# Optimization experiments

Hardware: AMD Instinct MI355X
Metric: run time of the kernel (lower is better)

## Reference

```python
import jax, jax.numpy as jnp
import numpy as np

D_MODEL = 1024
N_HEADS = 16
D_K = D_MODEL // N_HEADS


def _rope_sin_cos(seq_len, d_k, dtype):
    inv_freq = 1.0 / (10000.0 ** (jnp.arange(0, d_k, 2, dtype=jnp.float32) / d_k))
    pos = jnp.arange(seq_len, dtype=jnp.float32)[:, None]          # [S,1]
    ang = pos * inv_freq[None, :]                                   # [S,d_k/2]
    sin = jnp.concatenate([jnp.sin(ang), jnp.sin(ang)], axis=-1)    # [S,d_k]
    cos = jnp.concatenate([jnp.cos(ang), jnp.cos(ang)], axis=-1)
    return sin.astype(dtype), cos.astype(dtype)


def _rotate_half(x):
    x1, x2 = jnp.split(x, 2, axis=-1)
    return jnp.concatenate([-x2, x1], axis=-1)


def _apply_rope(x, sin, cos):
    # x: [B,H,S,d_k]; sin/cos: [S,d_k] broadcast over B,H
    return x * cos[None, None] + _rotate_half(x) * sin[None, None]


def setup_inputs() -> dict:
    key = jax.random.key(0)
    ks = jax.random.split(key, 8)
    B, S = 2, 2048
    s = 1.0 / np.sqrt(D_MODEL)
    return {
        "query": jax.random.normal(ks[0], (B, S, D_MODEL), jnp.float32),
        "key": jax.random.normal(ks[1], (B, S, D_MODEL), jnp.float32),
        "value": jax.random.normal(ks[2], (B, S, D_MODEL), jnp.float32),
        "Wq": jax.random.normal(ks[3], (D_MODEL, D_MODEL), jnp.float32) * s,
        "Wk": jax.random.normal(ks[4], (D_MODEL, D_MODEL), jnp.float32) * s,
        "Wv": jax.random.normal(ks[5], (D_MODEL, D_MODEL), jnp.float32) * s,
        "Wo": jax.random.normal(ks[6], (D_MODEL, D_MODEL), jnp.float32) * s,
        "bo": jnp.zeros((D_MODEL,), jnp.float32),
    }


def reference(query, key, value, Wq, Wk, Wv, Wo, bo):
    B, Sq, _ = query.shape
    Sk = key.shape[1]
    # projections; torch Linear: x @ W.T (here W stored as [out,in])
    Q = (query @ Wq.T).reshape(B, Sq, N_HEADS, D_K).transpose(0, 2, 1, 3)
    K = (key @ Wk.T).reshape(B, Sk, N_HEADS, D_K).transpose(0, 2, 1, 3)
    V = (value @ Wv.T).reshape(B, Sk, N_HEADS, D_K).transpose(0, 2, 1, 3)
    sin_q, cos_q = _rope_sin_cos(Sq, D_K, Q.dtype)
    sin_k, cos_k = _rope_sin_cos(Sk, D_K, K.dtype)
    Q = _apply_rope(Q, sin_q, cos_q)
    K = _apply_rope(K, sin_k, cos_k)
    scores = jnp.einsum("bhqd,bhkd->bhqk", Q, K) / jnp.sqrt(jnp.asarray(D_K, Q.dtype))
    attn = jax.nn.softmax(scores, axis=-1)
    ctx = jnp.einsum("bhqk,bhkd->bhqd", attn, V)
    ctx = ctx.transpose(0, 2, 1, 3).reshape(B, Sq, D_MODEL)
    out = ctx @ Wo.T + bo
    return out, attn
```

## Files before the change

kernel.cpp:

```cpp
#include <hip/hip_runtime.h>
#include <cmath>

#define BB 2
#define SS 2048
#define DMODEL 1024
#define NHEADS 16
#define DK 64
#define BSR (BB*SS)

typedef float f32x4 __attribute__((ext_vector_type(4)));
typedef short s16x8 __attribute__((ext_vector_type(8)));
typedef unsigned short ushort_t;
#define MFMA_BF16 __builtin_amdgcn_mfma_f32_16x16x32_bf16

__device__ __forceinline__ unsigned short f2bf(float x) {
    unsigned int u = __float_as_uint(x);
    unsigned int r = u + 0x7FFFu + ((u >> 16) & 1u);
    return (unsigned short)(r >> 16);
}
__device__ __forceinline__ float bf2f(unsigned short h) {
    return __uint_as_float(((unsigned int)h) << 16);
}
__device__ __forceinline__ unsigned int pk2(float lo, float hi) {
    return (unsigned int)f2bf(lo) | ((unsigned int)f2bf(hi) << 16);
}

__device__ __forceinline__ size_t qk_idx(int bh, int s, int d) {
    return ((((size_t)bh * 128 + (s >> 4)) * 2 + (d >> 5)) * 4 + ((d >> 3) & 3)) * 128
           + (size_t)((s & 15) * 8 + (d & 7));
}
__device__ __forceinline__ size_t v_idx(int bh, int s, int d) {
    return ((((size_t)bh * 64 + (s >> 5)) * 4 + (d >> 4)) * 4 + ((s >> 3) & 3)) * 128
           + (size_t)((d & 15) * 8 + (s & 7));
}

__global__ __launch_bounds__(256)
void split_tab(const float* __restrict__ q, const float* __restrict__ k,
               const float* __restrict__ v, const float* __restrict__ wq,
               const float* __restrict__ wk, const float* __restrict__ wv,
               const float* __restrict__ wo,
               ushort_t* qsh, ushort_t* qsl, ushort_t* ksh, ushort_t* ksl,
               ushort_t* vsh, ushort_t* vsl,
               ushort_t* wqh, ushort_t* wql, ushort_t* wkh, ushort_t* wkl,
               ushort_t* wvh, ushort_t* wvl, ushort_t* woh, ushort_t* wol,
               float2* __restrict__ tab)
{
    int blk = blockIdx.x;
    if (blk >= 8192) {
        const int t = (blk - 8192) * 256 + threadIdx.x;
        const int s = t >> 5, j = t & 31;
        const double l2 = 13.287712379549449 / 32.0;
        const float invf = (float)exp2(-(double)j * l2);
        const float ang = (float)s * invf;
        tab[t] = make_float2(cosf(ang), sinf(ang));
        return;
    }
    const float* src; ushort_t* dh; ushort_t* dl;
    if      (blk < 2048) { src = q;  dh = qsh; dl = qsl; }
    else if (blk < 4096) { src = k;  dh = ksh; dl = ksl; blk -= 2048; }
    else if (blk < 6144) { src = v;  dh = vsh; dl = vsl; blk -= 4096; }
    else if (blk < 6656) { src = wq; dh = wqh; dl = wql; blk -= 6144; }
    else if (blk < 7168) { src = wk; dh = wkh; dl = wkl; blk -= 6656; }
    else if (blk < 7680) { src = wv; dh = wvh; dl = wvl; blk -= 7168; }
    else                 { src = wo; dh = woh; dl = wol; blk -= 7680; }
    const size_t off = (size_t)blk * 2048 + threadIdx.x * 8;
    float4 a = *reinterpret_cast<const float4*>(src + off);
    float4 b = *reinterpret_cast<const float4*>(src + off + 4);
    float xs[8] = {a.x, a.y, a.z, a.w, b.x, b.y, b.z, b.w};
    s16x8 hi, lo;
#pragma unroll
    for (int i = 0; i < 8; ++i) {
        unsigned short h = f2bf(xs[i]);
        hi[i] = (short)h;
        lo[i] = (short)f2bf(xs[i] - bf2f(h));
    }
    *reinterpret_cast<s16x8*>(dh + off) = hi;
    *reinterpret_cast<s16x8*>(dl + off) = lo;
}

__global__ __launch_bounds__(256)
void qkv_gemm(const ushort_t* __restrict__ qsh, const ushort_t* __restrict__ qsl,
              const ushort_t* __restrict__ ksh, const ushort_t* __restrict__ ksl,
              const ushort_t* __restrict__ vsh, const ushort_t* __restrict__ vsl,
              const ushort_t* __restrict__ wqh, const ushort_t* __restrict__ wql,
              const ushort_t* __restrict__ wkh, const ushort_t* __restrict__ wkl,
              const ushort_t* __restrict__ wvh, const ushort_t* __restrict__ wvl,
              ushort_t* __restrict__ Qhi, ushort_t* __restrict__ Qlo,
              ushort_t* __restrict__ Khi, ushort_t* __restrict__ Klo,
              ushort_t* __restrict__ Vt,
              const float2* __restrict__ tab)
{
    __shared__ __align__(16) ushort_t smAh[128 * 64];
    __shared__ __align__(16) ushort_t smAl[128 * 64];
    __shared__ __align__(16) ushort_t smBh[64 * 64];
    __shared__ __align__(16) ushort_t smBl[64 * 64];

    const int tid = threadIdx.x;
    const int lane = tid & 63;
    const int w = tid >> 6;
    const int lane16 = lane & 15;
    const int grp = (lane >> 4) & 3;
    const int m0 = blockIdx.y * 128;
    const int n0 = blockIdx.x * 64;
    const int z  = blockIdx.z;
    const int K = 1024;

    const ushort_t* Ah = (z == 0) ? vsh : ((z == 1) ? qsh : ksh);
    const ushort_t* Al = (z == 0) ? vsl : ((z == 1) ? qsl : ksl);
    const ushort_t* Bh = (z == 0) ? wvh : ((z == 1) ? wqh : wkh);
    const ushort_t* Bl = (z == 0) ? wvl : ((z == 1) ? wql : wkl);

    f32x4 acc[2][4];
#pragma unroll
    for (int a = 0; a < 2; ++a)
#pragma unroll
        for (int e = 0; e < 4; ++e) acc[a][e] = (f32x4){0.f, 0.f, 0.f, 0.f};

    for (int k0 = 0; k0 < K; k0 += 64) {
#pragma unroll
        for (int i = 0; i < 4; ++i) {
            const int c = tid + 256 * i;
            const int row = c >> 3, gs = c & 7;
            const int dst = row * 64 + ((gs ^ (row & 7)) * 8);
            const size_t src = (size_t)(m0 + row) * K + k0 + gs * 8;
            *reinterpret_cast<s16x8*>(&smAh[dst]) = *reinterpret_cast<const s16x8*>(&Ah[src]);
            *reinterpret_cast<s16x8*>(&smAl[dst]) = *reinterpret_cast<const s16x8*>(&Al[src]);
        }
#pragma unroll
        for (int i = 0; i < 2; ++i) {
            const int c = tid + 256 * i;
            const int row = c >> 3, gs = c & 7;
            const int dst = row * 64 + ((gs ^ (row & 7)) * 8);
            const size_t src = (size_t)(n0 + row) * K + k0 + gs * 8;
            *reinterpret_cast<s16x8*>(&smBh[dst]) = *reinterpret_cast<const s16x8*>(&Bh[src]);
            *reinterpret_cast<s16x8*>(&smBl[dst]) = *reinterpret_cast<const s16x8*>(&Bl[src]);
        }
        __syncthreads();
#pragma unroll
        for (int ks = 0; ks < 2; ++ks) {
            const int slotk = ks * 4 + grp;
            s16x8 afh[2], afl[2], bfh[4], bfl[4];
#pragma unroll
            for (int mt = 0; mt < 2; ++mt) {
                const int row = w * 32 + mt * 16 + lane16;
                const int off = row * 64 + ((slotk ^ (row & 7)) * 8);
                afh[mt] = *reinterpret_cast<const s16x8*>(&smAh[off]);
                afl[mt] = *reinterpret_cast<const s16x8*>(&smAl[off]);
            }
#pragma unroll
            for (int nt = 0; nt < 4; ++nt) {
                const int row = nt * 16 + lane16;
                const int off = row * 64 + ((slotk ^ (row & 7)) * 8);
                bfh[nt] = *reinterpret_cast<const s16x8*>(&smBh[off]);
                bfl[nt] = *reinterpret_cast<const s16x8*>(&smBl[off]);
            }
#pragma unroll
            for (int mt = 0; mt < 2; ++mt)
#pragma unroll
                for (int nt = 0; nt < 4; ++nt) {
                    acc[mt][nt] = MFMA_BF16(afh[mt], bfl[nt], acc[mt][nt], 0, 0, 0);
                    acc[mt][nt] = MFMA_BF16(afl[mt], bfh[nt], acc[mt][nt], 0, 0, 0);
                    acc[mt][nt] = MFMA_BF16(afh[mt], bfh[nt], acc[mt][nt], 0, 0, 0);
                }
        }
        __syncthreads();
    }

    const int hh = blockIdx.x;
    if (z == 0) {
#pragma unroll
        for (int mt = 0; mt < 2; ++mt)
#pragma unroll
            for (int r = 0; r < 4; ++r) {
                const int m = m0 + w * 32 + mt * 16 + grp * 4 + r;
                const int b = m >> 11, s = m & (SS - 1);
                const int bh = b * 16 + hh;
#pragma unroll
                for (int nt = 0; nt < 4; ++nt) {
                    const int d = nt * 16 + lane16;
                    Vt[v_idx(bh, s, d)] = f2bf(acc[mt][nt][r]);
                }
            }
    } else {
        ushort_t* O1 = (z == 1) ? Qhi : Khi;
        ushort_t* O2 = (z == 1) ? Qlo : Klo;
#pragma unroll
        for (int mt = 0; mt < 2; ++mt)
#pragma unroll
            for (int r = 0; r < 4; ++r) {
                const int m = m0 + w * 32 + mt * 16 + grp * 4 + r;
                const int b = m >> 11, s = m & (SS - 1);
                const int bh = b * 16 + hh;
#pragma unroll
                for (int ntp = 0; ntp < 2; ++ntp) {
                    const int j = ntp * 16 + lane16;
                    const float2 cs = tab[s * 32 + j];
                    const float x1 = acc[mt][ntp][r], x2 = acc[mt][ntp + 2][r];
                    const float r1 = x1 * cs.x - x2 * cs.y;
                    const float r2 = x2 * cs.x + x1 * cs.y;
                    const size_t i1 = qk_idx(bh, s, j);
                    const size_t i2 = qk_idx(bh, s, j + 32);
                    const unsigned short h1 = f2bf(r1);
                    O1[i1] = h1;  O2[i1] = f2bf(r1 - bf2f(h1));
                    const unsigned short h2 = f2bf(r2);
                    O1[i2] = h2;  O2[i2] = f2bf(r2 - bf2f(h2));
                }
            }
    }
}

__global__ __launch_bounds__(256)
void gemm_out(const ushort_t* __restrict__ Ah, const ushort_t* __restrict__ Al,
              const ushort_t* __restrict__ Bh, const ushort_t* __restrict__ Bl,
              float* __restrict__ outF, const float* __restrict__ bias)
{
    __shared__ __align__(16) ushort_t smAh[128 * 64];
    __shared__ __align__(16) ushort_t smAl[128 * 64];
    __shared__ __align__(16) ushort_t smBh[64 * 64];
    __shared__ __align__(16) ushort_t smBl[64 * 64];

    const int tid = threadIdx.x;
    const int lane = tid & 63;
    const int w = tid >> 6;
    const int lane16 = lane & 15;
    const int grp = (lane >> 4) & 3;
    const int m0 = blockIdx.y * 128;
    const int n0 = blockIdx.x * 64;
    const int K = 1024;

    f32x4 acc[2][4];
#pragma unroll
    for (int a = 0; a < 2; ++a)
#pragma unroll
        for (int e = 0; e < 4; ++e) acc[a][e] = (f32x4){0.f, 0.f, 0.f, 0.f};

    for (int k0 = 0; k0 < K; k0 += 64) {
#pragma unroll
        for (int i = 0; i < 4; ++i) {
            const int c = tid + 256 * i;
            const int row = c >> 3, gs = c & 7;
            const int dst = row * 64 + ((gs ^ (row & 7)) * 8);
            const size_t src = (size_t)(m0 + row) * K + k0 + gs * 8;
            *reinterpret_cast<s16x8*>(&smAh[dst]) = *reinterpret_cast<const s16x8*>(&Ah[src]);
            *reinterpret_cast<s16x8*>(&smAl[dst]) = *reinterpret_cast<const s16x8*>(&Al[src]);
        }
#pragma unroll
        for (int i = 0; i < 2; ++i) {
            const int c = tid + 256 * i;
            const int row = c >> 3, gs = c & 7;
            const int dst = row * 64 + ((gs ^ (row & 7)) * 8);
            const size_t src = (size_t)(n0 + row) * K + k0 + gs * 8;
            *reinterpret_cast<s16x8*>(&smBh[dst]) = *reinterpret_cast<const s16x8*>(&Bh[src]);
            *reinterpret_cast<s16x8*>(&smBl[dst]) = *reinterpret_cast<const s16x8*>(&Bl[src]);
        }
        __syncthreads();
#pragma unroll
        for (int ks = 0; ks < 2; ++ks) {
            const int slotk = ks * 4 + grp;
            s16x8 afh[2], afl[2], bfh[4], bfl[4];
#pragma unroll
            for (int mt = 0; mt < 2; ++mt) {
                const int row = w * 32 + mt * 16 + lane16;
                const int off = row * 64 + ((slotk ^ (row & 7)) * 8);
                afh[mt] = *reinterpret_cast<const s16x8*>(&smAh[off]);
                afl[mt] = *reinterpret_cast<const s16x8*>(&smAl[off]);
            }
#pragma unroll
            for (int nt = 0; nt < 4; ++nt) {
                const int row = nt * 16 + lane16;
                const int off = row * 64 + ((slotk ^ (row & 7)) * 8);
                bfh[nt] = *reinterpret_cast<const s16x8*>(&smBh[off]);
                bfl[nt] = *reinterpret_cast<const s16x8*>(&smBl[off]);
            }
#pragma unroll
            for (int mt = 0; mt < 2; ++mt)
#pragma unroll
                for (int nt = 0; nt < 4; ++nt) {
                    acc[mt][nt] = MFMA_BF16(afh[mt], bfl[nt], acc[mt][nt], 0, 0, 0);
                    acc[mt][nt] = MFMA_BF16(afl[mt], bfh[nt], acc[mt][nt], 0, 0, 0);
                    acc[mt][nt] = MFMA_BF16(afh[mt], bfh[nt], acc[mt][nt], 0, 0, 0);
                }
        }
        __syncthreads();
    }

#pragma unroll
    for (int mt = 0; mt < 2; ++mt)
#pragma unroll
        for (int r = 0; r < 4; ++r) {
            const int m = m0 + w * 32 + mt * 16 + grp * 4 + r;
#pragma unroll
            for (int nt = 0; nt < 4; ++nt) {
                const int n = n0 + nt * 16 + lane16;
                outF[(size_t)m * 1024 + n] = acc[mt][nt][r] + bias[n];
            }
        }
}

#define SCALE_L2E 0.180336879f

__global__ __launch_bounds__(1024, 4)
void attn_v6(const ushort_t* __restrict__ Qf_h, const ushort_t* __restrict__ Qf_l,
             const ushort_t* __restrict__ Kf_h, const ushort_t* __restrict__ Kf_l,
             const ushort_t* __restrict__ Vf,
             float* __restrict__ attn, ushort_t* __restrict__ ctxh, ushort_t* __restrict__ ctxl)
{
    __shared__ __align__(16) float slots[8][32][68];
    __shared__ float lsum[16][32];
    __shared__ float rinvS[32];

    const int tid = threadIdx.x;
    const int lane = tid & 63;
    const int w = tid >> 6;
    const int lane16 = lane & 15;
    const int grp = lane >> 4;

    const int bid = blockIdx.x;
    const int idx = bid >> 3;
    const int bh = (bid & 7) * 4 + (idx >> 6);
    const int q0 = (idx & 63) * 32;

    s16x8 qh[2][2], ql[2][2];
#pragma unroll
    for (int qt = 0; qt < 2; ++qt) {
        const size_t qb = ((size_t)(bh * 128 + (q0 >> 4) + qt) * 2) * 512 + lane * 8;
        qh[qt][0] = *reinterpret_cast<const s16x8*>(Qf_h + qb);
        qh[qt][1] = *reinterpret_cast<const s16x8*>(Qf_h + qb + 512);
        ql[qt][0] = *reinterpret_cast<const s16x8*>(Qf_l + qb);
        ql[qt][1] = *reinterpret_cast<const s16x8*>(Qf_l + qb + 512);
    }

    f32x4 p[8][2];
#pragma unroll
    for (int kt = 0; kt < 8; ++kt) {
        const size_t kb = ((size_t)(bh * 128 + w * 8 + kt) * 2) * 512 + lane * 8;
        const s16x8 kh0 = *reinterpret_cast<const s16x8*>(Kf_h + kb);
        const s16x8 kh1 = *reinterpret_cast<const s16x8*>(Kf_h + kb + 512);
        const s16x8 kl0 = *reinterpret_cast<const s16x8*>(Kf_l + kb);
        const s16x8 kl1 = *reinterpret_cast<const s16x8*>(Kf_l + kb + 512);
#pragma unroll
        for (int qt = 0; qt < 2; ++qt) {
            f32x4 t = {0.f, 0.f, 0.f, 0.f};
            t = MFMA_BF16(kh0, ql[qt][0], t, 0, 0, 0);
            t = MFMA_BF16(kh1, ql[qt][1], t, 0, 0, 0);
            t = MFMA_BF16(kl0, qh[qt][0], t, 0, 0, 0);
            t = MFMA_BF16(kl1, qh[qt][1], t, 0, 0, 0);
            t = MFMA_BF16(kh0, qh[qt][0], t, 0, 0, 0);
            t = MFMA_BF16(kh1, qh[qt][1], t, 0, 0, 0);
            p[kt][qt] = t;
        }
    }

    float lq[2] = {0.f, 0.f};
#pragma unroll
    for (int kt = 0; kt < 8; ++kt)
#pragma unroll
        for (int qt = 0; qt < 2; ++qt)
#pragma unroll
            for (int r = 0; r < 4; ++r) {
                const float e = exp2f(p[kt][qt][r] * SCALE_L2E);
                p[kt][qt][r] = e;
                lq[qt] += e;
            }
#pragma unroll
    for (int qt = 0; qt < 2; ++qt) {
        lq[qt] += __shfl_xor(lq[qt], 16, 64);
        lq[qt] += __shfl_xor(lq[qt], 32, 64);
    }
    if (grp == 0) {
        lsum[w][lane16]      = lq[0];
        lsum[w][16 + lane16] = lq[1];
    }
    __syncthreads();
    float tot0 = 0.f, tot1 = 0.f;
#pragma unroll
    for (int w2 = 0; w2 < 16; ++w2) {
        tot0 += lsum[w2][lane16];
        tot1 += lsum[w2][16 + lane16];
    }
    const float rinv[2] = {1.0f / tot0, 1.0f / tot1};
    if (w == 0 && grp == 0) {
        rinvS[lane16]      = rinv[0];
        rinvS[16 + lane16] = rinv[1];
    }

#pragma unroll
    for (int qt = 0; qt < 2; ++qt) {
        const size_t arow = ((size_t)bh * SS + q0 + qt * 16 + lane16) * SS + w * 128 + grp * 4;
#pragma unroll
        for (int kt = 0; kt < 8; ++kt) {
            f32x4 v4;
            v4[0] = p[kt][qt][0] * rinv[qt]; v4[1] = p[kt][qt][1] * rinv[qt];
            v4[2] = p[kt][qt][2] * rinv[qt]; v4[3] = p[kt][qt][3] * rinv[qt];
            __builtin_nontemporal_store(v4, reinterpret_cast<f32x4*>(&attn[arow + kt * 16]));
        }
    }

    f32x4 acc[4][2];
#pragma unroll
    for (int dt = 0; dt < 4; ++dt) {
        acc[dt][0] = (f32x4){0.f, 0.f, 0.f, 0.f};
        acc[dt][1] = (f32x4){0.f, 0.f, 0.f, 0.f};
    }
    const int src0 = lane16 + ((grp & 1) << 5);
    const int src1 = src0 + 16;
    const bool sel = (grp >> 1) != 0;
#pragma unroll
    for (int kc = 0; kc < 4; ++kc) {
        s16x8 bfr[2];
#pragma unroll
        for (int qt = 0; qt < 2; ++qt) {
            const unsigned int A0 = pk2(p[2*kc][qt][0],   p[2*kc][qt][1]);
            const unsigned int A1 = pk2(p[2*kc][qt][2],   p[2*kc][qt][3]);
            const unsigned int B0 = pk2(p[2*kc+1][qt][0], p[2*kc+1][qt][1]);
            const unsigned int B1 = pk2(p[2*kc+1][qt][2], p[2*kc+1][qt][3]);
            const unsigned int d0a = (unsigned int)__shfl((int)A0, src0, 64);
            const unsigned int d0b = (unsigned int)__shfl((int)B0, src0, 64);
            const unsigned int d1a = (unsigned int)__shfl((int)A1, src0, 64);
            const unsigned int d1b = (unsigned int)__shfl((int)B1, src0, 64);
            const unsigned int d2a = (unsigned int)__shfl((int)A0, src1, 64);
            const unsigned int d2b = (unsigned int)__shfl((int)B0, src1, 64);
            const unsigned int d3a = (unsigned int)__shfl((int)A1, src1, 64);
            const unsigned int d3b = (unsigned int)__shfl((int)B1, src1, 64);
            union { unsigned int u[4]; s16x8 v; } bu;
            bu.u[0] = sel ? d0b : d0a;
            bu.u[1] = sel ? d1b : d1a;
            bu.u[2] = sel ? d2b : d2a;
            bu.u[3] = sel ? d3b : d3a;
            bfr[qt] = bu.v;
        }
#pragma unroll
        for (int dt = 0; dt < 4; ++dt) {
            const s16x8 vf = *reinterpret_cast<const s16x8*>(
                &Vf[((size_t)(bh * 64 + w * 4 + kc) * 4 + dt) * 512 + lane * 8]);
            acc[dt][0] = MFMA_BF16(vf, bfr[0], acc[dt][0], 0, 0, 0);
            acc[dt][1] = MFMA_BF16(vf, bfr[1], acc[dt][1], 0, 0, 0);
        }
    }

    if (w >= 8) {
        float* slot = &slots[w - 8][0][0];
#pragma unroll
        for (int dt = 0; dt < 4; ++dt)
#pragma unroll
            for (int qt = 0; qt < 2; ++qt) {
                f32x4 v4;
                v4[0] = acc[dt][qt][0]; v4[1] = acc[dt][qt][1];
                v4[2] = acc[dt][qt][2]; v4[3] = acc[dt][qt][3];
                *reinterpret_cast<f32x4*>(&slot[(qt * 16 + lane16) * 68 + dt * 16 + grp * 4]) = v4;
            }
    }
    __syncthreads();
    if (w < 8) {
        float* slot = &slots[w][0][0];
#pragma unroll
        for (int dt = 0; dt < 4; ++dt)
#pragma unroll
            for (int qt = 0; qt < 2; ++qt) {
                f32x4* pp = reinterpret_cast<f32x4*>(&slot[(qt * 16 + lane16) * 68 + dt * 16 + grp * 4]);
                f32x4 o = *pp;
                o[0] += acc[dt][qt][0]; o[1] += acc[dt][qt][1];
                o[2] += acc[dt][qt][2]; o[3] += acc[dt][qt][3];
                *pp = o;
            }
    }
    __syncthreads();

    {
        const int b = bh >> 4, h = bh & 15;
        const int q = tid >> 5;
        const int dp = (tid & 31) * 2;
        float s0 = 0.f, s1 = 0.f;
#pragma unroll
        for (int s = 0; s < 8; ++s) {
            const float2 v = *reinterpret_cast<const float2*>(&slots[s][q][dp]);
            s0 += v.x; s1 += v.y;
        }
        const float rv = rinvS[q];
        s0 *= rv; s1 *= rv;
        const size_t co = ((size_t)b * SS + q0 + q) * DMODEL + h * DK + dp;
        const unsigned short h0 = f2bf(s0);
        const unsigned short l0 = f2bf(s0 - bf2f(h0));
        const unsigned short h1 = f2bf(s1);
        const unsigned short l1 = f2bf(s1 - bf2f(h1));
        *reinterpret_cast<unsigned int*>(ctxh + co) = (unsigned int)h0 | ((unsigned int)h1 << 16);
        *reinterpret_cast<unsigned int*>(ctxl + co) = (unsigned int)l0 | ((unsigned int)l1 << 16);
    }
}

extern "C" void kernel_launch(void* const* d_in, const int* in_sizes, int n_in,
                              void* d_out, int out_size, void* d_ws, size_t ws_size,
                              hipStream_t stream)
{
    const float* query = (const float*)d_in[0];
    const float* key   = (const float*)d_in[1];
    const float* value = (const float*)d_in[2];
    const float* Wq    = (const float*)d_in[3];
    const float* Wk    = (const float*)d_in[4];
    const float* Wv    = (const float*)d_in[5];
    const float* Wo    = (const float*)d_in[6];
    const float* bo    = (const float*)d_in[7];

    float* out   = (float*)d_out;
    float* attnO = out + (size_t)BSR * DMODEL;

    const size_t NPROJ = (size_t)BSR * DMODEL;
    const size_t NW    = (size_t)DMODEL * DMODEL;

    char* p = (char*)d_ws;
    float2* tab = (float2*)p;                 p += 1 << 20;
    ushort_t* qsh = (ushort_t*)p;             p += NPROJ * 2;
    ushort_t* qsl = (ushort_t*)p;             p += NPROJ * 2;
    ushort_t* ksh = (ushort_t*)p;             p += NPROJ * 2;
    ushort_t* ksl = (ushort_t*)p;             p += NPROJ * 2;
    ushort_t* vsh = (ushort_t*)p;             p += NPROJ * 2;
    ushort_t* vsl = (ushort_t*)p;             p += NPROJ * 2;
    ushort_t* wqh = (ushort_t*)p;             p += NW * 2;
    ushort_t* wql = (ushort_t*)p;             p += NW * 2;
    ushort_t* wkh = (ushort_t*)p;             p += NW * 2;
    ushort_t* wkl = (ushort_t*)p;             p += NW * 2;
    ushort_t* wvh = (ushort_t*)p;             p += NW * 2;
    ushort_t* wvl = (ushort_t*)p;             p += NW * 2;
    ushort_t* woh = (ushort_t*)p;             p += NW * 2;
    ushort_t* wol = (ushort_t*)p;             p += NW * 2;
    ushort_t* Vt  = (ushort_t*)p;             p += NPROJ * 2;
    ushort_t* Qhi = vsh; ushort_t* Qlo = vsl;
    ushort_t* Khi = qsh; ushort_t* Klo = qsl;
    ushort_t* ctxhC = ksh; ushort_t* ctxlC = ksl;

    split_tab<<<8448, 256, 0, stream>>>(query, key, value, Wq, Wk, Wv, Wo,
                                        qsh, qsl, ksh, ksl, vsh, vsl,
                                        wqh, wql, wkh, wkl, wvh, wvl, woh, wol, tab);

    ushort_t* QhiX = (ushort_t*)p;            p += NPROJ * 2;
    ushort_t* QloX = (ushort_t*)p;            p += NPROJ * 2;
    ushort_t* KhiX = (ushort_t*)p;            p += NPROJ * 2;
    ushort_t* KloX = (ushort_t*)p;            p += NPROJ * 2;

    qkv_gemm<<<dim3(16, 32, 3), 256, 0, stream>>>(qsh, qsl, ksh, ksl, vsh, vsl,
                                                  wqh, wql, wkh, wkl, wvh, wvl,
                                                  QhiX, QloX, KhiX, KloX, Vt, tab);

    attn_v6<<<dim3(2048), 1024, 0, stream>>>(QhiX, QloX, KhiX, KloX, Vt, attnO, ctxhC, ctxlC);

    gemm_out<<<dim3(16, 32), 256, 0, stream>>>(ctxhC, ctxlC, woh, wol, out, bo);
}
```

Measured before the change: 346.7 us.

## Drop split-precision for V projection and keep softmax probabilities packed bf16

In the QKV projection kernel, the V slice skips loading low-order bf16 parts and their two correction MFMAs, computing V with hi parts only. In the attention kernel, exponentials are computed immediately after each score tile and stored as packed bf16 pairs instead of fp32 vectors, reducing register usage. The attention probabilities written out are now derived from bf16-rounded exponentials, and V loses the split-precision accuracy, trading accuracy for fewer MFMAs, loads and registers.

```diff
diff --git a/kernel.cpp b/kernel.cpp
--- a/kernel.cpp
+++ b/kernel.cpp
@@ -104,6 +104,7 @@
     const int n0 = blockIdx.x * 64;
     const int z  = blockIdx.z;
     const int K = 1024;
+    const bool split = (z != 0);
 
     const ushort_t* Ah = (z == 0) ? vsh : ((z == 1) ? qsh : ksh);
     const ushort_t* Al = (z == 0) ? vsl : ((z == 1) ? qsl : ksl);
@@ -124,7 +125,8 @@
             const int dst = row * 64 + ((gs ^ (row & 7)) * 8);
             const size_t src = (size_t)(m0 + row) * K + k0 + gs * 8;
             *reinterpret_cast<s16x8*>(&smAh[dst]) = *reinterpret_cast<const s16x8*>(&Ah[src]);
-            *reinterpret_cast<s16x8*>(&smAl[dst]) = *reinterpret_cast<const s16x8*>(&Al[src]);
+            if (split)
+                *reinterpret_cast<s16x8*>(&smAl[dst]) = *reinterpret_cast<const s16x8*>(&Al[src]);
         }
 #pragma unroll
         for (int i = 0; i < 2; ++i) {
@@ -133,7 +135,8 @@
             const int dst = row * 64 + ((gs ^ (row & 7)) * 8);
             const size_t src = (size_t)(n0 + row) * K + k0 + gs * 8;
             *reinterpret_cast<s16x8*>(&smBh[dst]) = *reinterpret_cast<const s16x8*>(&Bh[src]);
-            *reinterpret_cast<s16x8*>(&smBl[dst]) = *reinterpret_cast<const s16x8*>(&Bl[src]);
+            if (split)
+                *reinterpret_cast<s16x8*>(&smBl[dst]) = *reinterpret_cast<const s16x8*>(&Bl[src]);
         }
         __syncthreads();
 #pragma unroll
@@ -145,21 +148,23 @@
                 const int row = w * 32 + mt * 16 + lane16;
                 const int off = row * 64 + ((slotk ^ (row & 7)) * 8);
                 afh[mt] = *reinterpret_cast<const s16x8*>(&smAh[off]);
-                afl[mt] = *reinterpret_cast<const s16x8*>(&smAl[off]);
+                if (split) afl[mt] = *reinterpret_cast<const s16x8*>(&smAl[off]);
             }
 #pragma unroll
             for (int nt = 0; nt < 4; ++nt) {
                 const int row = nt * 16 + lane16;
                 const int off = row * 64 + ((slotk ^ (row & 7)) * 8);
                 bfh[nt] = *reinterpret_cast<const s16x8*>(&smBh[off]);
-                bfl[nt] = *reinterpret_cast<const s16x8*>(&smBl[off]);
+                if (split) bfl[nt] = *reinterpret_cast<const s16x8*>(&smBl[off]);
             }
 #pragma unroll
             for (int mt = 0; mt < 2; ++mt)
 #pragma unroll
                 for (int nt = 0; nt < 4; ++nt) {
-                    acc[mt][nt] = MFMA_BF16(afh[mt], bfl[nt], acc[mt][nt], 0, 0, 0);
-                    acc[mt][nt] = MFMA_BF16(afl[mt], bfh[nt], acc[mt][nt], 0, 0, 0);
+                    if (split) {
+                        acc[mt][nt] = MFMA_BF16(afh[mt], bfl[nt], acc[mt][nt], 0, 0, 0);
+                        acc[mt][nt] = MFMA_BF16(afl[mt], bfh[nt], acc[mt][nt], 0, 0, 0);
+                    }
                     acc[mt][nt] = MFMA_BF16(afh[mt], bfh[nt], acc[mt][nt], 0, 0, 0);
                 }
         }
@@ -300,7 +305,7 @@
 #define SCALE_L2E 0.180336879f
 
 __global__ __launch_bounds__(1024, 4)
-void attn_v6(const ushort_t* __restrict__ Qf_h, const ushort_t* __restrict__ Qf_l,
+void attn_v8(const ushort_t* __restrict__ Qf_h, const ushort_t* __restrict__ Qf_l,
              const ushort_t* __restrict__ Kf_h, const ushort_t* __restrict__ Kf_l,
              const ushort_t* __restrict__ Vf,
              float* __restrict__ attn, ushort_t* __restrict__ ctxh, ushort_t* __restrict__ ctxl)
@@ -330,7 +335,8 @@
         ql[qt][1] = *reinterpret_cast<const s16x8*>(Qf_l + qb + 512);
     }
 
-    f32x4 p[8][2];
+    unsigned int pp[8][2][2];
+    float lq[2] = {0.f, 0.f};
 #pragma unroll
     for (int kt = 0; kt < 8; ++kt) {
         const size_t kb = ((size_t)(bh * 128 + w * 8 + kt) * 2) * 512 + lane * 8;
@@ -347,21 +353,16 @@
             t = MFMA_BF16(kl1, qh[qt][1], t, 0, 0, 0);
             t = MFMA_BF16(kh0, qh[qt][0], t, 0, 0, 0);
             t = MFMA_BF16(kh1, qh[qt][1], t, 0, 0, 0);
-            p[kt][qt] = t;
-        }
-    }
-
-    float lq[2] = {0.f, 0.f};
-#pragma unroll
-    for (int kt = 0; kt < 8; ++kt)
-#pragma unroll
-        for (int qt = 0; qt < 2; ++qt)
-#pragma unroll
-            for (int r = 0; r < 4; ++r) {
-                const float e = exp2f(p[kt][qt][r] * SCALE_L2E);
-                p[kt][qt][r] = e;
-                lq[qt] += e;
-            }
+            const float e0 = exp2f(t[0] * SCALE_L2E);
+            const float e1 = exp2f(t[1] * SCALE_L2E);
+            const float e2 = exp2f(t[2] * SCALE_L2E);
+            const float e3 = exp2f(t[3] * SCALE_L2E);
+            lq[qt] += e0 + e1 + e2 + e3;
+            pp[kt][qt][0] = pk2(e0, e1);
+            pp[kt][qt][1] = pk2(e2, e3);
+        }
+    }
+
 #pragma unroll
     for (int qt = 0; qt < 2; ++qt) {
         lq[qt] += __shfl_xor(lq[qt], 16, 64);
@@ -389,9 +390,13 @@
         const size_t arow = ((size_t)bh * SS + q0 + qt * 16 + lane16) * SS + w * 128 + grp * 4;
 #pragma unroll
         for (int kt = 0; kt < 8; ++kt) {
+            const unsigned int u0 = pp[kt][qt][0];
+            const unsigned int u1 = pp[kt][qt][1];
             f32x4 v4;
-            v4[0] = p[kt][qt][0] * rinv[qt]; v4[1] = p[kt][qt][1] * rinv[qt];
-            v4[2] = p[kt][qt][2] * rinv[qt]; v4[3] = p[kt][qt][3] * rinv[qt];
+            v4[0] = __uint_as_float(u0 << 16) * rinv[qt];
+            v4[1] = __uint_as_float(u0 & 0xffff0000u) * rinv[qt];
+            v4[2] = __uint_as_float(u1 << 16) * rinv[qt];
+            v4[3] = __uint_as_float(u1 & 0xffff0000u) * rinv[qt];
             __builtin_nontemporal_store(v4, reinterpret_cast<f32x4*>(&attn[arow + kt * 16]));
         }
     }
@@ -410,10 +415,10 @@
         s16x8 bfr[2];
 #pragma unroll
         for (int qt = 0; qt < 2; ++qt) {
-            const unsigned int A0 = pk2(p[2*kc][qt][0],   p[2*kc][qt][1]);
-            const unsigned int A1 = pk2(p[2*kc][qt][2],   p[2*kc][qt][3]);
-            const unsigned int B0 = pk2(p[2*kc+1][qt][0], p[2*kc+1][qt][1]);
-            const unsigned int B1 = pk2(p[2*kc+1][qt][2], p[2*kc+1][qt][3]);
+            const unsigned int A0 = pp[2 * kc][qt][0];
+            const unsigned int A1 = pp[2 * kc][qt][1];
+            const unsigned int B0 = pp[2 * kc + 1][qt][0];
+            const unsigned int B1 = pp[2 * kc + 1][qt][1];
             const unsigned int d0a = (unsigned int)__shfl((int)A0, src0, 64);
             const unsigned int d0b = (unsigned int)__shfl((int)B0, src0, 64);
             const unsigned int d1a = (unsigned int)__shfl((int)A1, src0, 64);
@@ -457,11 +462,11 @@
         for (int dt = 0; dt < 4; ++dt)
 #pragma unroll
             for (int qt = 0; qt < 2; ++qt) {
-                f32x4* pp = reinterpret_cast<f32x4*>(&slot[(qt * 16 + lane16) * 68 + dt * 16 + grp * 4]);
-                f32x4 o = *pp;
+                f32x4* pq = reinterpret_cast<f32x4*>(&slot[(qt * 16 + lane16) * 68 + dt * 16 + grp * 4]);
+                f32x4 o = *pq;
                 o[0] += acc[dt][qt][0]; o[1] += acc[dt][qt][1];
                 o[2] += acc[dt][qt][2]; o[3] += acc[dt][qt][3];
-                *pp = o;
+                *pq = o;
             }
     }
     __syncthreads();
@@ -524,24 +529,22 @@
     ushort_t* woh = (ushort_t*)p;             p += NW * 2;
     ushort_t* wol = (ushort_t*)p;             p += NW * 2;
     ushort_t* Vt  = (ushort_t*)p;             p += NPROJ * 2;
-    ushort_t* Qhi = vsh; ushort_t* Qlo = vsl;
-    ushort_t* Khi = qsh; ushort_t* Klo = qsl;
-    ushort_t* ctxhC = ksh; ushort_t* ctxlC = ksl;
-
-    split_tab<<<8448, 256, 0, stream>>>(query, key, value, Wq, Wk, Wv, Wo,
-                                        qsh, qsl, ksh, ksl, vsh, vsl,
-                                        wqh, wql, wkh, wkl, wvh, wvl, woh, wol, tab);
-
+    ushort_t* ctxhC = ksh;
+    ushort_t* ctxlC = ksl;
     ushort_t* QhiX = (ushort_t*)p;            p += NPROJ * 2;
     ushort_t* QloX = (ushort_t*)p;            p += NPROJ * 2;
     ushort_t* KhiX = (ushort_t*)p;            p += NPROJ * 2;
     ushort_t* KloX = (ushort_t*)p;            p += NPROJ * 2;
 
+    split_tab<<<8448, 256, 0, stream>>>(query, key, value, Wq, Wk, Wv, Wo,
+                                        qsh, qsl, ksh, ksl, vsh, vsl,
+                                        wqh, wql, wkh, wkl, wvh, wvl, woh, wol, tab);
+
     qkv_gemm<<<dim3(16, 32, 3), 256, 0, stream>>>(qsh, qsl, ksh, ksl, vsh, vsl,
                                                   wqh, wql, wkh, wkl, wvh, wvl,
                                                   QhiX, QloX, KhiX, KloX, Vt, tab);
 
-    attn_v6<<<dim3(2048), 1024, 0, stream>>>(QhiX, QloX, KhiX, KloX, Vt, attnO, ctxhC, ctxlC);
+    attn_v8<<<dim3(2048), 1024, 0, stream>>>(QhiX, QloX, KhiX, KloX, Vt, attnO, ctxhC, ctxlC);
 
     gemm_out<<<dim3(16, 32), 256, 0, stream>>>(ctxhC, ctxlC, woh, wol, out, bo);
 }
```

Measured after the change: 339.0 us, median of 2. -2.2%, faster.
